# Kernel tuning notes

Hardware: AMD Instinct MI355X
Metric: run time of the kernel (lower is better)

The kernel has to match this reference:

```python
import jax, jax.numpy as jnp
import numpy as np

# Config (matches init_kwargs)
B, S, D = 1, 2048, 1024
H, KH, HD = 8, 2, 128          # n_heads, n_kv_heads, head_dim
R = 64                         # lora_rank
WINDOWS = [256, 512, 1024]
GLOBAL = 128
SCALE = HD ** -0.5
N_REP = H // KH


def _lora(x, w, a, b):
    # y = x @ w.T + (x @ A.T) @ B.T / rank
    return x @ w.T + (x @ a.T) @ b.T * (1.0 / R)


def _rope(x, cs):
    # x: [b, s, h, d]; cs: [s, d//2, 2] (cos, sin) -> complex rotation per pair
    b, s, h, d = x.shape
    xr = x.reshape(b, s, h, d // 2, 2)
    cos = cs[None, :, None, :, 0]
    sin = cs[None, :, None, :, 1]
    x1, x2 = xr[..., 0], xr[..., 1]
    out = jnp.stack([x1 * cos - x2 * sin, x1 * sin + x2 * cos], axis=-1)
    return out.reshape(b, s, h, d)


def _sparse_masks(q_len, k_len):
    aq = jnp.arange(q_len)
    ak = jnp.arange(k_len)
    diff = jnp.abs(ak[None, :] - aq[:, None])
    m = jnp.stack([(diff <= w // 2).astype(jnp.float32) for w in WINDOWS])  # [nw,q,k]
    return m.at[:, :, :GLOBAL].set(1.0)


def setup_inputs() -> dict:
    key = jax.random.key(0)
    ks = jax.random.split(key, 16)
    init = lambda k, shape: (jax.random.normal(k, shape, jnp.float32) * 0.02)
    return {
        "x": jax.random.normal(ks[0], (B, S, D), jnp.float32),
        "freqs_cis": jax.random.normal(ks[1], (S, HD // 2, 2), jnp.float32),
        "wq_w": init(ks[2], (H * HD, D)), "wq_a": init(ks[3], (R, D)), "wq_b": init(ks[4], (H * HD, R)),
        "wk_w": init(ks[5], (KH * HD, D)), "wk_a": init(ks[6], (R, D)), "wk_b": init(ks[7], (KH * HD, R)),
        "wv_w": init(ks[8], (KH * HD, D)), "wv_a": init(ks[9], (R, D)), "wv_b": init(ks[10], (KH * HD, R)),
        "wo_w": init(ks[11], (D, H * HD)), "wo_a": init(ks[12], (R, H * HD)), "wo_b": init(ks[13], (D, R)),
        "scale_weights": jnp.ones((len(WINDOWS),), jnp.float32),
        "start_pos": 0,
    }


def reference(x, freqs_cis, wq_w, wq_a, wq_b, wk_w, wk_a, wk_b, wv_w, wv_a, wv_b,
              wo_w, wo_a, wo_b, scale_weights, start_pos):
    bsz, seqlen, _ = x.shape
    xq = _lora(x, wq_w, wq_a, wq_b).reshape(bsz, seqlen, H, HD)
    xk = _lora(x, wk_w, wk_a, wk_b).reshape(bsz, seqlen, KH, HD)
    xv = _lora(x, wv_w, wv_a, wv_b).reshape(bsz, seqlen, KH, HD)
    cs = freqs_cis[start_pos:start_pos + seqlen]
    xq = _rope(xq, cs)
    xk = _rope(xk, cs)
    # no kv_cache: key/value = current xk/xv, repeated for GQA
    key = jnp.repeat(xk, N_REP, axis=2)    # [b,k,H,hd]
    value = jnp.repeat(xv, N_REP, axis=2)
    scores = jnp.einsum('bqhd,bkhd->bhqk', xq, key) * SCALE       # [b,H,q,k]
    masks = _sparse_masks(seqlen, key.shape[1])                    # [nw,q,k]
    multi_scores = scores[:, None] - (1.0 - masks)[None, :, None] * 10000.0  # [b,nw,H,q,k]
    multi_attn = jax.nn.softmax(multi_scores, axis=-1)
    w = jax.nn.softmax(scale_weights)[None, :, None, None, None]
    attn = (multi_attn * w).sum(axis=1)                            # [b,H,q,k]
    out = jnp.einsum('bhqk,bkhd->bqhd', attn, value).reshape(bsz, seqlen, H * HD)
    return _lora(out, wo_w, wo_a, wo_b)
```

## Files before the change

### kernel.cpp

```cpp
#include <hip/hip_runtime.h>
#include <hip/hip_bf16.h>
#include <cstdint>

#define S_LEN   2048
#define DMODEL  1024
#define NHEAD   8
#define HD      128
#define QSCALE  (0.08838834764831845f * 1.4426950408889634f)
#define THR2    11.5416f

typedef __attribute__((ext_vector_type(8))) short  bf16x8;
typedef __attribute__((ext_vector_type(4))) float  f32x4;

typedef __attribute__((address_space(1))) const unsigned int gu32;
typedef __attribute__((address_space(3))) unsigned int       lu32;

static __device__ __forceinline__ unsigned short f2bf(float x) {
  union { float f; unsigned u; } c; c.f = x;
  unsigned u = c.u + 0x7fff + ((c.u >> 16) & 1);
  return (unsigned short)(u >> 16);
}
static __device__ __forceinline__ f32x4 fz4() {
  f32x4 v; v[0] = 0.f; v[1] = 0.f; v[2] = 0.f; v[3] = 0.f; return v;
}

__global__ __launch_bounds__(256) void xcvt_kernel(
    const float* __restrict__ X, unsigned short* __restrict__ Xb)
{
  const int i = blockIdx.x * 256 + threadIdx.x;
  const float4 v = ((const float4*)X)[i];
  ushort4 o;
  o.x = f2bf(v.x); o.y = f2bf(v.y); o.z = f2bf(v.z); o.w = f2bf(v.w);
  ((ushort4*)Xb)[i] = o;
}

__global__ __launch_bounds__(256) void fuse_all_kernel(
    const float* __restrict__ wq_w, const float* __restrict__ wq_a, const float* __restrict__ wq_b,
    const float* __restrict__ wk_w, const float* __restrict__ wk_a, const float* __restrict__ wk_b,
    const float* __restrict__ wv_w, const float* __restrict__ wv_a, const float* __restrict__ wv_b,
    const float* __restrict__ wo_w, const float* __restrict__ wo_a, const float* __restrict__ wo_b,
    unsigned short* __restrict__ Wqkv, unsigned short* __restrict__ Wo)
{
  __shared__ float bs[64];
  const int t = threadIdx.x;
  const int o = blockIdx.x;
  const float *w, *a, *b; unsigned short* out; int ol;
  if (o < 1024)      { w = wq_w; a = wq_a; b = wq_b; out = Wqkv;              ol = o; }
  else if (o < 1280) { w = wk_w; a = wk_a; b = wk_b; out = Wqkv + 1024*1024;  ol = o - 1024; }
  else if (o < 1536) { w = wv_w; a = wv_a; b = wv_b; out = Wqkv + 1280*1024;  ol = o - 1280; }
  else               { w = wo_w; a = wo_a; b = wo_b; out = Wo;                ol = o - 1536; }
  if (t < 64) bs[t] = b[(size_t)ol * 64 + t];
  __syncthreads();
  float4 acc = {0.f, 0.f, 0.f, 0.f};
#pragma unroll 8
  for (int r = 0; r < 64; ++r) {
    const float4 av = *(const float4*)(a + (size_t)r * 1024 + t * 4);
    const float br = bs[r];
    acc.x += br * av.x; acc.y += br * av.y; acc.z += br * av.z; acc.w += br * av.w;
  }
  const float4 wv = *(const float4*)(w + (size_t)ol * 1024 + t * 4);
  ushort4 ov;
  ov.x = f2bf(wv.x + acc.x * 0.015625f);
  ov.y = f2bf(wv.y + acc.y * 0.015625f);
  ov.z = f2bf(wv.z + acc.z * 0.015625f);
  ov.w = f2bf(wv.w + acc.w * 0.015625f);
  *(ushort4*)(out + (size_t)ol * 1024 + t * 4) = ov;
}

template<int HEADMAJOR>
__global__ __launch_bounds__(256) void gemm_bf16(
    const unsigned short* __restrict__ A, const unsigned short* __restrict__ B,
    float* __restrict__ Y, int M, int N, int K)
{
  __shared__ __align__(16) unsigned short lds[2][(64 + 128) * 64];
  const int t = threadIdx.x;
  const int l = t & 63, wid = t >> 6;
  const int lr = l & 15, lq = l >> 4;
  const int m0 = blockIdx.y * 64, n0 = blockIdx.x * 128;
  const int wm = (wid >> 1) * 32, wn = (wid & 1) * 64;

  f32x4 acc[2][4];
#pragma unroll
  for (int i = 0; i < 2; ++i)
#pragma unroll
    for (int j = 0; j < 4; ++j) acc[i][j] = fz4();

  auto stage = [&](int buf, int k0) {
#pragma unroll
    for (int i = 0; i < 6; ++i) {
      const int ch = wid * 6 + i;
      const unsigned short* src;
      unsigned short* dst;
      int row;
      if (ch < 8) {
        row = ch * 8 + (l >> 3);
        src = A + (size_t)(m0 + row) * K + k0;
        dst = &lds[buf][ch * 512];
      } else {
        const int bh = ch - 8;
        row = bh * 8 + (l >> 3);
        src = B + (size_t)(n0 + row) * K + k0;
        dst = &lds[buf][4096 + bh * 512];
      }
      const int cg = (l & 7) ^ (row & 7);
      __builtin_amdgcn_global_load_lds((gu32*)(src + cg * 8), (lu32*)dst, 16, 0, 0);
    }
  };

  auto compute = [&](int buf) {
    const unsigned short* la = &lds[buf][0];
    const unsigned short* lb = &lds[buf][4096];
    bf16x8 af[2][2], bfr[4][2];
#pragma unroll
    for (int mi = 0; mi < 2; ++mi)
#pragma unroll
      for (int c = 0; c < 2; ++c) {
        const int row = wm + mi * 16 + lr;
        const int ck = (c * 4 + lq) ^ (row & 7);
        af[mi][c] = *(const bf16x8*)(la + row * 64 + ck * 8);
      }
#pragma unroll
    for (int nj = 0; nj < 4; ++nj)
#pragma unroll
      for (int c = 0; c < 2; ++c) {
        const int row = wn + nj * 16 + lr;
        const int ck = (c * 4 + lq) ^ (row & 7);
        bfr[nj][c] = *(const bf16x8*)(lb + row * 64 + ck * 8);
      }
#pragma unroll
    for (int c = 0; c < 2; ++c)
#pragma unroll
      for (int mi = 0; mi < 2; ++mi)
#pragma unroll
        for (int nj = 0; nj < 4; ++nj)
          acc[mi][nj] = __builtin_amdgcn_mfma_f32_16x16x32_bf16(
              af[mi][c], bfr[nj][c], acc[mi][nj], 0, 0, 0);
  };

  const int NT = K >> 6;
  stage(0, 0);
  int cur = 0;
#pragma unroll 1
  for (int kt = 0; kt < NT; ++kt) {
    __syncthreads();
    if (kt + 1 < NT) stage(cur ^ 1, (kt + 1) << 6);
    compute(cur);
    cur ^= 1;
  }

#pragma unroll
  for (int mi = 0; mi < 2; ++mi)
#pragma unroll
    for (int nj = 0; nj < 4; ++nj)
#pragma unroll
      for (int r = 0; r < 4; ++r) {
        const int row = m0 + wm + mi * 16 + lq * 4 + r;
        const int col = n0 + wn + nj * 16 + lr;
        if (HEADMAJOR)
          Y[(((size_t)(col >> 7) * M + row) << 7) + (col & 127)] = acc[mi][nj][r];
        else
          Y[(size_t)row * N + col] = acc[mi][nj][r];
      }
}

__global__ __launch_bounds__(256) void rope_cvt_kernel(
    const float* __restrict__ QKV, const float* __restrict__ fc,
    const int* __restrict__ sp,
    unsigned short* __restrict__ Qb, unsigned short* __restrict__ Kb)
{
  const int idx = blockIdx.x * 256 + threadIdx.x;
  const int i   = idx & 63;
  const int s   = (idx >> 6) & (S_LEN - 1);
  const int sec = idx >> 17;
  const float2 v  = *(const float2*)(QKV + ((size_t)sec * S_LEN + s) * 128 + 2 * i);
  const float2 cs = *(const float2*)(fc + (size_t)(sp[0] + s) * 128 + 2 * i);
  float xr = v.x * cs.x - v.y * cs.y;
  float yr = v.x * cs.y + v.y * cs.x;
  if (sec < 8) { xr *= QSCALE; yr *= QSCALE; }
  const unsigned w = (unsigned)f2bf(xr) | ((unsigned)f2bf(yr) << 16);
  if (sec < 8)
    ((unsigned*)Qb)[(((size_t)sec * S_LEN + s) * 128 + 2 * i) >> 1] = w;
  else
    ((unsigned*)Kb)[(((size_t)(sec - 8) * S_LEN + s) * 128 + 2 * i) >> 1] = w;
}

__global__ __launch_bounds__(256) void vtrans_kernel(
    const float* __restrict__ QKV, unsigned short* __restrict__ Vt)
{
  __shared__ float T[64][68];
  const int t = threadIdx.x;
  const int b = blockIdx.x;
  const int dt = b & 1, st = (b >> 1) & 31, kh = b >> 6;
  const int s0 = st * 64, d0 = dt * 64;
  const float* src = QKV + ((size_t)(10 + kh) * S_LEN + s0) * 128 + d0;
  const int row = t >> 4, c4 = (t & 15) * 4;
#pragma unroll
  for (int i = 0; i < 4; ++i) {
    const float4 v = *(const float4*)(src + (size_t)(row + i * 16) * 128 + c4);
    *(float4*)&T[row + i * 16][c4] = v;
  }
  __syncthreads();
  const int dl = t >> 2, s4 = (t & 3) * 16;
  unsigned short* dst = Vt + ((size_t)(kh * 128 + d0 + dl)) * S_LEN + s0 + s4;
#pragma unroll
  for (int half = 0; half < 2; ++half) {
    union { unsigned short u[8]; uint4 q; } o;
#pragma unroll
    for (int jj = 0; jj < 8; ++jj) o.u[jj] = f2bf(T[s4 + half * 8 + jj][dl]);
    *(uint4*)(dst + half * 8) = o.q;
  }
}

__global__ __launch_bounds__(128, 2) void attn_kernel(
    const unsigned short* __restrict__ Qb,
    const unsigned short* __restrict__ Kb,
    const unsigned short* __restrict__ Vt,
    const float* __restrict__ swp,
    unsigned short* __restrict__ AO)
{
  __shared__ __align__(16) unsigned short P[2][512];
  __shared__ __align__(16) float OS[6144];
  __shared__ float ST[3][16];
  __shared__ float MW;

  const int t   = threadIdx.x;
  const int wid = t >> 6;
  const int l   = t & 63;
  const int lr  = l & 15, lq = l >> 4;
  const int h   = blockIdx.y;
  const int q0  = blockIdx.x << 4;
  const int kvh = h >> 2;

  const unsigned short* Kp = Kb + (size_t)kvh * S_LEN * 128;
  const unsigned short* Vp = Vt + (size_t)kvh * 128 * S_LEN;

  bf16x8 qf[4];
#pragma unroll
  for (int c = 0; c < 4; ++c)
    qf[c] = *(const bf16x8*)(Qb + ((size_t)(h * S_LEN + q0 + lr)) * 128 + c * 32 + lq * 8);

  f32x4 o0[8], o1[8], o2[8];
#pragma unroll
  for (int i = 0; i < 8; ++i) { o0[i] = fz4(); o1[i] = fz4(); o2[i] = fz4(); }
  float sA[4], sB[4], sC[4];
#pragma unroll
  for (int r = 0; r < 4; ++r) { sA[r] = 0.f; sB[r] = 0.f; sC[r] = 0.f; }
  float M = -1e30f;

  const int t0w = (q0 >= 512) ? ((q0 - 512) >> 5) : 0;
  const int t1w = min(63, (q0 + 527) >> 5);
  int nA, base;
  if (t0w < 4) { nA = 0; base = 0; }
  else         { nA = 4; base = t0w; }
  const int n  = nA + t1w - base + 1;
  const int nh = n >> 1;
  const int jb = wid ? nh : 0;
  const int je = wid ? n  : nh;

#pragma unroll 1
  for (int j = jb; j < je; ++j) {
    const int tt = (j < nA) ? j : (base + j - nA);
    const int k0 = tt << 5;

    f32x4 s0 = fz4(), s1 = fz4();
#pragma unroll
    for (int c = 0; c < 4; ++c) {
      bf16x8 kf0 = *(const bf16x8*)(Kp + (size_t)(k0 + lr) * 128 + c * 32 + lq * 8);
      s0 = __builtin_amdgcn_mfma_f32_16x16x32_bf16(qf[c], kf0, s0, 0, 0, 0);
    }
#pragma unroll
    for (int c = 0; c < 4; ++c) {
      bf16x8 kf1 = *(const bf16x8*)(Kp + (size_t)(k0 + 16 + lr) * 128 + c * 32 + lq * 8);
      s1 = __builtin_amdgcn_mfma_f32_16x16x32_bf16(qf[c], kf1, s1, 0, 0, 0);
    }

    const int dminT = k0 - (q0 + 15);
    const int dmaxT = k0 + 31 - q0;
    const int aminT = (dminT <= 0 && dmaxT >= 0) ? 0 : min(::abs(dminT), ::abs(dmaxT));
    const int amaxT = max(::abs(dminT), ::abs(dmaxT));
    const int bminT = aminT <= 128 ? 0 : aminT <= 256 ? 1 : aminT <= 512 ? 2 : 3;
    const int bmaxT = amaxT <= 128 ? 0 : amaxT <= 256 ? 1 : amaxT <= 512 ? 2 : 3;
    const bool unifA = (k0 < 128);
    const bool unif  = unifA || (bminT == bmaxT);
    const int  ucls  = unifA ? 0 : bminT;

    float lm = fmaxf(s0[0], s1[0]);
#pragma unroll
    for (int r = 1; r < 4; ++r) lm = fmaxf(lm, fmaxf(s0[r], s1[r]));
    if (__any(lm > M + THR2)) {
      float wm = lm;
      wm = fmaxf(wm, __shfl_xor(wm, 1, 64));
      wm = fmaxf(wm, __shfl_xor(wm, 2, 64));
      wm = fmaxf(wm, __shfl_xor(wm, 4, 64));
      wm = fmaxf(wm, __shfl_xor(wm, 8, 64));
      wm = fmaxf(wm, __shfl_xor(wm, 16, 64));
      wm = fmaxf(wm, __shfl_xor(wm, 32, 64));
      const float Mn = fmaxf(M, wm);
      const float sc = __builtin_amdgcn_exp2f(M - Mn);
      M = Mn;
#pragma unroll
      for (int r = 0; r < 4; ++r) { sA[r] *= sc; sB[r] *= sc; sC[r] *= sc; }
#pragma unroll
      for (int db = 0; db < 8; ++db) { o0[db] *= sc; o1[db] *= sc; o2[db] *= sc; }
    }

    float p0[4], p1[4];
    int c0[4], c1[4];
#pragma unroll
    for (int r = 0; r < 4; ++r) {
      float e0 = __builtin_amdgcn_exp2f(s0[r] - M);
      float e1 = __builtin_amdgcn_exp2f(s1[r] - M);
      if (unif) {
        c0[r] = ucls; c1[r] = ucls;
        if (ucls == 0)      sA[r] += e0 + e1;
        else if (ucls == 1) sB[r] += e0 + e1;
        else                sC[r] += e0 + e1;
      } else {
        const int q  = q0 + lq * 4 + r;
        const int a0 = ::abs(k0 + lr - q);
        const int a1 = ::abs(k0 + 16 + lr - q);
        c0[r] = a0 <= 128 ? 0 : a0 <= 256 ? 1 : a0 <= 512 ? 2 : 3;
        c1[r] = a1 <= 128 ? 0 : a1 <= 256 ? 1 : a1 <= 512 ? 2 : 3;
        if (c0[r] == 3) e0 = 0.f;
        if (c1[r] == 3) e1 = 0.f;
        if (c0[r] == 0) sA[r] += e0; else if (c0[r] == 1) sB[r] += e0; else if (c0[r] == 2) sC[r] += e0;
        if (c1[r] == 0) sA[r] += e1; else if (c1[r] == 1) sB[r] += e1; else if (c1[r] == 2) sC[r] += e1;
      }
      p0[r] = e0; p1[r] = e1;
    }

    bf16x8 vf[8];
#pragma unroll
    for (int db = 0; db < 8; ++db)
      vf[db] = *(const bf16x8*)(Vp + (size_t)(db * 16 + lr) * S_LEN + k0 + lq * 8);

    if (unif) {
#pragma unroll
      for (int r = 0; r < 4; ++r) {
        const int q = lq * 4 + r;
        P[wid][q * 32 + (((lr >> 3) ^ r) << 3) + (lr & 7)]        = f2bf(p0[r]);
        P[wid][q * 32 + ((((16 + lr) >> 3) ^ r) << 3) + (lr & 7)] = f2bf(p1[r]);
      }
      const bf16x8 pa = *(const bf16x8*)&P[wid][lr * 32 + ((lq ^ (lr & 3)) << 3)];
      if (ucls == 0) {
#pragma unroll
        for (int db = 0; db < 8; ++db)
          o0[db] = __builtin_amdgcn_mfma_f32_16x16x32_bf16(pa, vf[db], o0[db], 0, 0, 0);
      } else if (ucls == 1) {
#pragma unroll
        for (int db = 0; db < 8; ++db)
          o1[db] = __builtin_amdgcn_mfma_f32_16x16x32_bf16(pa, vf[db], o1[db], 0, 0, 0);
      } else {
#pragma unroll
        for (int db = 0; db < 8; ++db)
          o2[db] = __builtin_amdgcn_mfma_f32_16x16x32_bf16(pa, vf[db], o2[db], 0, 0, 0);
      }
    } else {
#pragma unroll 1
      for (int pass = 0; pass < 2; ++pass) {
        const int cc = (pass == 0) ? bminT : bmaxT;
        if (cc == 3) continue;
#pragma unroll
        for (int r = 0; r < 4; ++r) {
          const int q = lq * 4 + r;
          const float u0 = (c0[r] == cc) ? p0[r] : 0.f;
          const float u1 = (c1[r] == cc) ? p1[r] : 0.f;
          P[wid][q * 32 + (((lr >> 3) ^ r) << 3) + (lr & 7)]        = f2bf(u0);
          P[wid][q * 32 + ((((16 + lr) >> 3) ^ r) << 3) + (lr & 7)] = f2bf(u1);
        }
        const bf16x8 pa = *(const bf16x8*)&P[wid][lr * 32 + ((lq ^ (lr & 3)) << 3)];
        if (cc == 0) {
#pragma unroll
          for (int db = 0; db < 8; ++db)
            o0[db] = __builtin_amdgcn_mfma_f32_16x16x32_bf16(pa, vf[db], o0[db], 0, 0, 0);
        } else if (cc == 1) {
#pragma unroll
          for (int db = 0; db < 8; ++db)
            o1[db] = __builtin_amdgcn_mfma_f32_16x16x32_bf16(pa, vf[db], o1[db], 0, 0, 0);
        } else {
#pragma unroll
          for (int db = 0; db < 8; ++db)
            o2[db] = __builtin_amdgcn_mfma_f32_16x16x32_bf16(pa, vf[db], o2[db], 0, 0, 0);
        }
      }
    }
  }

#pragma unroll
  for (int r = 0; r < 4; ++r) {
    sA[r] += __shfl_xor(sA[r], 1, 64); sA[r] += __shfl_xor(sA[r], 2, 64);
    sA[r] += __shfl_xor(sA[r], 4, 64); sA[r] += __shfl_xor(sA[r], 8, 64);
    sB[r] += __shfl_xor(sB[r], 1, 64); sB[r] += __shfl_xor(sB[r], 2, 64);
    sB[r] += __shfl_xor(sB[r], 4, 64); sB[r] += __shfl_xor(sB[r], 8, 64);
    sC[r] += __shfl_xor(sC[r], 1, 64); sC[r] += __shfl_xor(sC[r], 2, 64);
    sC[r] += __shfl_xor(sC[r], 4, 64); sC[r] += __shfl_xor(sC[r], 8, 64);
  }

  if (wid == 1) {
    if (l == 0) MW = M;
    if (lr == 0) {
#pragma unroll
      for (int r = 0; r < 4; ++r) {
        ST[0][lq * 4 + r] = sA[r];
        ST[1][lq * 4 + r] = sB[r];
        ST[2][lq * 4 + r] = sC[r];
      }
    }
#pragma unroll
    for (int db = 0; db < 8; ++db)
#pragma unroll
      for (int r = 0; r < 4; ++r) {
        OS[((0 * 8 + db) * 4 + r) * 64 + l] = o0[db][r];
        OS[((1 * 8 + db) * 4 + r) * 64 + l] = o1[db][r];
        OS[((2 * 8 + db) * 4 + r) * 64 + l] = o2[db][r];
      }
  }
  __syncthreads();
  if (wid == 1) return;

  {
    const float M1 = MW;
    const float Mn = fmaxf(M, M1);
    const float f0 = __builtin_amdgcn_exp2f(M - Mn);
    const float f1 = __builtin_amdgcn_exp2f(M1 - Mn);
#pragma unroll
    for (int r = 0; r < 4; ++r) {
      sA[r] = f0 * sA[r] + f1 * ST[0][lq * 4 + r];
      sB[r] = f0 * sB[r] + f1 * ST[1][lq * 4 + r];
      sC[r] = f0 * sC[r] + f1 * ST[2][lq * 4 + r];
    }
#pragma unroll
    for (int db = 0; db < 8; ++db)
#pragma unroll
      for (int r = 0; r < 4; ++r) {
        o0[db][r] = f0 * o0[db][r] + f1 * OS[((0 * 8 + db) * 4 + r) * 64 + l];
        o1[db][r] = f0 * o1[db][r] + f1 * OS[((1 * 8 + db) * 4 + r) * 64 + l];
        o2[db][r] = f0 * o2[db][r] + f1 * OS[((2 * 8 + db) * 4 + r) * 64 + l];
      }
  }

  const float w0 = swp[0], w1 = swp[1], w2 = swp[2];
  const float mw = fmaxf(w0, fmaxf(w1, w2));
  const float e0 = __expf(w0 - mw), e1 = __expf(w1 - mw), e2 = __expf(w2 - mw);
  const float inv = 1.f / (e0 + e1 + e2);
  const float g0 = e0 * inv, g1 = e1 * inv, g2 = e2 * inv;

#pragma unroll
  for (int r = 0; r < 4; ++r) {
    const float Z1 = sA[r], Z2 = Z1 + sB[r], Z3 = Z2 + sC[r];
    const float cC = g2 / Z3;
    const float cB = g1 / Z2 + cC;
    const float cA = g0 / Z1 + cB;
#pragma unroll
    for (int db = 0; db < 8; ++db)
      OS[(lq * 4 + r) * 132 + db * 16 + lr] =
          o0[db][r] * cA + o1[db][r] * cB + o2[db][r] * cC;
  }

  const int qr = l >> 2, dc = (l & 3) * 8;
  unsigned short* dst = AO + (size_t)(q0 + qr) * DMODEL + h * HD + dc;
#pragma unroll
  for (int j = 0; j < 4; ++j) {
    const float4 v0 = *(const float4*)&OS[qr * 132 + dc + j * 32];
    const float4 v1 = *(const float4*)&OS[qr * 132 + dc + j * 32 + 4];
    union { unsigned short u[8]; uint4 q4; } pk;
    pk.u[0] = f2bf(v0.x); pk.u[1] = f2bf(v0.y); pk.u[2] = f2bf(v0.z); pk.u[3] = f2bf(v0.w);
    pk.u[4] = f2bf(v1.x); pk.u[5] = f2bf(v1.y); pk.u[6] = f2bf(v1.z); pk.u[7] = f2bf(v1.w);
    *(uint4*)(dst + j * 32) = pk.q4;
  }
}

extern "C" void kernel_launch(void* const* d_in, const int* in_sizes, int n_in,
                              void* d_out, int out_size, void* d_ws, size_t ws_size,
                              hipStream_t stream) {
  const float* x    = (const float*)d_in[0];
  const float* fc   = (const float*)d_in[1];
  const float* wq_w = (const float*)d_in[2];
  const float* wq_a = (const float*)d_in[3];
  const float* wq_b = (const float*)d_in[4];
  const float* wk_w = (const float*)d_in[5];
  const float* wk_a = (const float*)d_in[6];
  const float* wk_b = (const float*)d_in[7];
  const float* wv_w = (const float*)d_in[8];
  const float* wv_a = (const float*)d_in[9];
  const float* wv_b = (const float*)d_in[10];
  const float* wo_w = (const float*)d_in[11];
  const float* wo_a = (const float*)d_in[12];
  const float* wo_b = (const float*)d_in[13];
  const float* sw   = (const float*)d_in[14];
  const int*   sp   = (const int*)d_in[15];
  float* out = (float*)d_out;

  char* wsb = (char*)d_ws;
  unsigned short* Wqkv = (unsigned short*)(wsb + 0);
  unsigned short* Wo   = (unsigned short*)(wsb + 3145728);
  unsigned short* Xbf  = (unsigned short*)(wsb + 5242880);
  float*          QKV  = (float*)(wsb + 9437184);
  unsigned short* Qb   = (unsigned short*)(wsb + 22020096);
  unsigned short* Kb   = (unsigned short*)(wsb + 26214400);
  unsigned short* Vt   = (unsigned short*)(wsb + 27262976);
  unsigned short* AO   = (unsigned short*)(wsb + 5242880);

  xcvt_kernel<<<2048, 256, 0, stream>>>(x, Xbf);
  fuse_all_kernel<<<2560, 256, 0, stream>>>(
      wq_w, wq_a, wq_b, wk_w, wk_a, wk_b, wv_w, wv_a, wv_b, wo_w, wo_a, wo_b,
      Wqkv, Wo);

  gemm_bf16<1><<<dim3(12, 32), 256, 0, stream>>>(Xbf, Wqkv, QKV, 2048, 1536, 1024);

  rope_cvt_kernel<<<5120, 256, 0, stream>>>(QKV, fc, sp, Qb, Kb);
  vtrans_kernel<<<128, 256, 0, stream>>>(QKV, Vt);

  attn_kernel<<<dim3(128, 8), 128, 0, stream>>>(Qb, Kb, Vt, sw, AO);

  gemm_bf16<0><<<dim3(8, 32), 256, 0, stream>>>(AO, Wo, out, 2048, 1024, 1024);
}
```

Measured before the change: 221.0 us.

## Two-pass attention with four-wave split, tiled LoRA fusion, smaller GEMM tiles

The attention kernel now uses four waves instead of two and runs two passes. The first pass finds the global row max and the per-window softmax denominators. The second pass folds the window-mixing coefficients into P, so only one O accumulator is kept instead of three, and a cheap LDS sum combines the waves. The LoRA weight-fusion kernel is re-tiled so each block computes a 64x128 output tile from shared-memory copies of A and B, cutting redundant global reads of A. The GEMM tile shrinks from 64x128 to 64x64 to launch more blocks; the costs are recomputing QK^T in the second pass and lower per-block reuse in the GEMM.

```diff
diff --git a/kernel.cpp b/kernel.cpp
--- a/kernel.cpp
+++ b/kernel.cpp
@@ -41,30 +41,62 @@
     const float* __restrict__ wo_w, const float* __restrict__ wo_a, const float* __restrict__ wo_b,
     unsigned short* __restrict__ Wqkv, unsigned short* __restrict__ Wo)
 {
-  __shared__ float bs[64];
-  const int t = threadIdx.x;
-  const int o = blockIdx.x;
-  const float *w, *a, *b; unsigned short* out; int ol;
-  if (o < 1024)      { w = wq_w; a = wq_a; b = wq_b; out = Wqkv;              ol = o; }
-  else if (o < 1280) { w = wk_w; a = wk_a; b = wk_b; out = Wqkv + 1024*1024;  ol = o - 1024; }
-  else if (o < 1536) { w = wv_w; a = wv_a; b = wv_b; out = Wqkv + 1280*1024;  ol = o - 1280; }
-  else               { w = wo_w; a = wo_a; b = wo_b; out = Wo;                ol = o - 1536; }
-  if (t < 64) bs[t] = b[(size_t)ol * 64 + t];
-  __syncthreads();
-  float4 acc = {0.f, 0.f, 0.f, 0.f};
-#pragma unroll 8
-  for (int r = 0; r < 64; ++r) {
-    const float4 av = *(const float4*)(a + (size_t)r * 1024 + t * 4);
-    const float br = bs[r];
-    acc.x += br * av.x; acc.y += br * av.y; acc.z += br * av.z; acc.w += br * av.w;
-  }
-  const float4 wv = *(const float4*)(w + (size_t)ol * 1024 + t * 4);
-  ushort4 ov;
-  ov.x = f2bf(wv.x + acc.x * 0.015625f);
-  ov.y = f2bf(wv.y + acc.y * 0.015625f);
-  ov.z = f2bf(wv.z + acc.z * 0.015625f);
-  ov.w = f2bf(wv.w + acc.w * 0.015625f);
-  *(ushort4*)(out + (size_t)ol * 1024 + t * 4) = ov;
+  __shared__ float bs[64][65];
+  __shared__ float as[16][132];
+  const int t  = threadIdx.x;
+  const int cb = blockIdx.x & 7, rb = blockIdx.x >> 3;
+  const int o0 = rb * 64;
+  const float *w, *a, *b; unsigned short* outp; int ob;
+  if (o0 < 1024)      { w = wq_w; a = wq_a; b = wq_b; outp = Wqkv;             ob = o0; }
+  else if (o0 < 1280) { w = wk_w; a = wk_a; b = wk_b; outp = Wqkv + 1024*1024; ob = o0 - 1024; }
+  else if (o0 < 1536) { w = wv_w; a = wv_a; b = wv_b; outp = Wqkv + 1280*1024; ob = o0 - 1280; }
+  else                { w = wo_w; a = wo_a; b = wo_b; outp = Wo;               ob = o0 - 1536; }
+
+#pragma unroll
+  for (int i = 0; i < 4; ++i) {
+    const int rr = (t >> 4) + i * 16, cc = (t & 15) * 4;
+    *(float4*)&bs[rr][cc] = *(const float4*)(b + (size_t)(ob + rr) * 64 + cc);
+  }
+
+  const int c0 = cb * 128;
+  const int tr = t >> 5;
+  const int co = (t & 31) * 4;
+  float4 ac[8];
+#pragma unroll
+  for (int i = 0; i < 8; ++i) ac[i] = {0.f, 0.f, 0.f, 0.f};
+
+#pragma unroll 1
+  for (int r0 = 0; r0 < 64; r0 += 16) {
+    __syncthreads();
+#pragma unroll
+    for (int i = 0; i < 2; ++i) {
+      const int rr = (t >> 5) + i * 8, cc = (t & 31) * 4;
+      *(float4*)&as[rr][cc] = *(const float4*)(a + (size_t)(r0 + rr) * 1024 + c0 + cc);
+    }
+    __syncthreads();
+#pragma unroll
+    for (int rr = 0; rr < 16; ++rr) {
+      const float4 av = *(const float4*)&as[rr][co];
+#pragma unroll
+      for (int ri = 0; ri < 8; ++ri) {
+        const float bv = bs[tr * 8 + ri][r0 + rr];
+        ac[ri].x += bv * av.x; ac[ri].y += bv * av.y;
+        ac[ri].z += bv * av.z; ac[ri].w += bv * av.w;
+      }
+    }
+  }
+
+#pragma unroll
+  for (int ri = 0; ri < 8; ++ri) {
+    const int row = tr * 8 + ri;
+    const float4 wv = *(const float4*)(w + (size_t)(ob + row) * 1024 + c0 + co);
+    ushort4 ov;
+    ov.x = f2bf(wv.x + ac[ri].x * 0.015625f);
+    ov.y = f2bf(wv.y + ac[ri].y * 0.015625f);
+    ov.z = f2bf(wv.z + ac[ri].z * 0.015625f);
+    ov.w = f2bf(wv.w + ac[ri].w * 0.015625f);
+    *(ushort4*)(outp + (size_t)(ob + row) * 1024 + c0 + co) = ov;
+  }
 }
 
 template<int HEADMAJOR>
@@ -72,23 +104,23 @@
     const unsigned short* __restrict__ A, const unsigned short* __restrict__ B,
     float* __restrict__ Y, int M, int N, int K)
 {
-  __shared__ __align__(16) unsigned short lds[2][(64 + 128) * 64];
+  __shared__ __align__(16) unsigned short lds[2][128 * 64];
   const int t = threadIdx.x;
   const int l = t & 63, wid = t >> 6;
   const int lr = l & 15, lq = l >> 4;
-  const int m0 = blockIdx.y * 64, n0 = blockIdx.x * 128;
-  const int wm = (wid >> 1) * 32, wn = (wid & 1) * 64;
-
-  f32x4 acc[2][4];
+  const int m0 = blockIdx.y * 64, n0 = blockIdx.x * 64;
+  const int wm = (wid >> 1) * 32, wn = (wid & 1) * 32;
+
+  f32x4 acc[2][2];
 #pragma unroll
   for (int i = 0; i < 2; ++i)
 #pragma unroll
-    for (int j = 0; j < 4; ++j) acc[i][j] = fz4();
+    for (int j = 0; j < 2; ++j) acc[i][j] = fz4();
 
   auto stage = [&](int buf, int k0) {
 #pragma unroll
-    for (int i = 0; i < 6; ++i) {
-      const int ch = wid * 6 + i;
+    for (int i = 0; i < 4; ++i) {
+      const int ch = wid * 4 + i;
       const unsigned short* src;
       unsigned short* dst;
       int row;
@@ -97,10 +129,9 @@
         src = A + (size_t)(m0 + row) * K + k0;
         dst = &lds[buf][ch * 512];
       } else {
-        const int bh = ch - 8;
-        row = bh * 8 + (l >> 3);
+        row = (ch - 8) * 8 + (l >> 3);
         src = B + (size_t)(n0 + row) * K + k0;
-        dst = &lds[buf][4096 + bh * 512];
+        dst = &lds[buf][ch * 512];
       }
       const int cg = (l & 7) ^ (row & 7);
       __builtin_amdgcn_global_load_lds((gu32*)(src + cg * 8), (lu32*)dst, 16, 0, 0);
@@ -110,7 +141,7 @@
   auto compute = [&](int buf) {
     const unsigned short* la = &lds[buf][0];
     const unsigned short* lb = &lds[buf][4096];
-    bf16x8 af[2][2], bfr[4][2];
+    bf16x8 af[2][2], bfr[2][2];
 #pragma unroll
     for (int mi = 0; mi < 2; ++mi)
 #pragma unroll
@@ -120,7 +151,7 @@
         af[mi][c] = *(const bf16x8*)(la + row * 64 + ck * 8);
       }
 #pragma unroll
-    for (int nj = 0; nj < 4; ++nj)
+    for (int nj = 0; nj < 2; ++nj)
 #pragma unroll
       for (int c = 0; c < 2; ++c) {
         const int row = wn + nj * 16 + lr;
@@ -132,7 +163,7 @@
 #pragma unroll
       for (int mi = 0; mi < 2; ++mi)
 #pragma unroll
-        for (int nj = 0; nj < 4; ++nj)
+        for (int nj = 0; nj < 2; ++nj)
           acc[mi][nj] = __builtin_amdgcn_mfma_f32_16x16x32_bf16(
               af[mi][c], bfr[nj][c], acc[mi][nj], 0, 0, 0);
   };
@@ -151,7 +182,7 @@
 #pragma unroll
   for (int mi = 0; mi < 2; ++mi)
 #pragma unroll
-    for (int nj = 0; nj < 4; ++nj)
+    for (int nj = 0; nj < 2; ++nj)
 #pragma unroll
       for (int r = 0; r < 4; ++r) {
         const int row = m0 + wm + mi * 16 + lq * 4 + r;
@@ -211,21 +242,20 @@
   }
 }
 
-__global__ __launch_bounds__(128, 2) void attn_kernel(
+__global__ __launch_bounds__(256, 3) void attn_kernel(
     const unsigned short* __restrict__ Qb,
     const unsigned short* __restrict__ Kb,
     const unsigned short* __restrict__ Vt,
     const float* __restrict__ swp,
     unsigned short* __restrict__ AO)
 {
-  __shared__ __align__(16) unsigned short P[2][512];
-  __shared__ __align__(16) float OS[6144];
-  __shared__ float ST[3][16];
-  __shared__ float MW;
+  __shared__ __align__(16) unsigned short P[4][512];
+  __shared__ float OS[4][32][65];
+  __shared__ float ST[4][3][16];
+  __shared__ float MB[4];
 
   const int t   = threadIdx.x;
-  const int wid = t >> 6;
-  const int l   = t & 63;
+  const int wid = t >> 6, l = t & 63;
   const int lr  = l & 15, lq = l >> 4;
   const int h   = blockIdx.y;
   const int q0  = blockIdx.x << 4;
@@ -238,14 +268,6 @@
 #pragma unroll
   for (int c = 0; c < 4; ++c)
     qf[c] = *(const bf16x8*)(Qb + ((size_t)(h * S_LEN + q0 + lr)) * 128 + c * 32 + lq * 8);
-
-  f32x4 o0[8], o1[8], o2[8];
-#pragma unroll
-  for (int i = 0; i < 8; ++i) { o0[i] = fz4(); o1[i] = fz4(); o2[i] = fz4(); }
-  float sA[4], sB[4], sC[4];
-#pragma unroll
-  for (int r = 0; r < 4; ++r) { sA[r] = 0.f; sB[r] = 0.f; sC[r] = 0.f; }
-  float M = -1e30f;
 
   const int t0w = (q0 >= 512) ? ((q0 - 512) >> 5) : 0;
   const int t1w = min(63, (q0 + 527) >> 5);
@@ -253,136 +275,83 @@
   if (t0w < 4) { nA = 0; base = 0; }
   else         { nA = 4; base = t0w; }
   const int n  = nA + t1w - base + 1;
-  const int nh = n >> 1;
-  const int jb = wid ? nh : 0;
-  const int je = wid ? n  : nh;
-
-#pragma unroll 1
-  for (int j = jb; j < je; ++j) {
-    const int tt = (j < nA) ? j : (base + j - nA);
-    const int k0 = tt << 5;
-
-    f32x4 s0 = fz4(), s1 = fz4();
-#pragma unroll
-    for (int c = 0; c < 4; ++c) {
-      bf16x8 kf0 = *(const bf16x8*)(Kp + (size_t)(k0 + lr) * 128 + c * 32 + lq * 8);
-      s0 = __builtin_amdgcn_mfma_f32_16x16x32_bf16(qf[c], kf0, s0, 0, 0, 0);
-    }
-#pragma unroll
-    for (int c = 0; c < 4; ++c) {
-      bf16x8 kf1 = *(const bf16x8*)(Kp + (size_t)(k0 + 16 + lr) * 128 + c * 32 + lq * 8);
-      s1 = __builtin_amdgcn_mfma_f32_16x16x32_bf16(qf[c], kf1, s1, 0, 0, 0);
-    }
-
-    const int dminT = k0 - (q0 + 15);
-    const int dmaxT = k0 + 31 - q0;
-    const int aminT = (dminT <= 0 && dmaxT >= 0) ? 0 : min(::abs(dminT), ::abs(dmaxT));
-    const int amaxT = max(::abs(dminT), ::abs(dmaxT));
-    const int bminT = aminT <= 128 ? 0 : aminT <= 256 ? 1 : aminT <= 512 ? 2 : 3;
-    const int bmaxT = amaxT <= 128 ? 0 : amaxT <= 256 ? 1 : amaxT <= 512 ? 2 : 3;
-    const bool unifA = (k0 < 128);
-    const bool unif  = unifA || (bminT == bmaxT);
-    const int  ucls  = unifA ? 0 : bminT;
-
-    float lm = fmaxf(s0[0], s1[0]);
-#pragma unroll
-    for (int r = 1; r < 4; ++r) lm = fmaxf(lm, fmaxf(s0[r], s1[r]));
-    if (__any(lm > M + THR2)) {
-      float wm = lm;
-      wm = fmaxf(wm, __shfl_xor(wm, 1, 64));
-      wm = fmaxf(wm, __shfl_xor(wm, 2, 64));
-      wm = fmaxf(wm, __shfl_xor(wm, 4, 64));
-      wm = fmaxf(wm, __shfl_xor(wm, 8, 64));
-      wm = fmaxf(wm, __shfl_xor(wm, 16, 64));
-      wm = fmaxf(wm, __shfl_xor(wm, 32, 64));
-      const float Mn = fmaxf(M, wm);
-      const float sc = __builtin_amdgcn_exp2f(M - Mn);
-      M = Mn;
-#pragma unroll
-      for (int r = 0; r < 4; ++r) { sA[r] *= sc; sB[r] *= sc; sC[r] *= sc; }
-#pragma unroll
-      for (int db = 0; db < 8; ++db) { o0[db] *= sc; o1[db] *= sc; o2[db] *= sc; }
-    }
-
-    float p0[4], p1[4];
-    int c0[4], c1[4];
-#pragma unroll
-    for (int r = 0; r < 4; ++r) {
-      float e0 = __builtin_amdgcn_exp2f(s0[r] - M);
-      float e1 = __builtin_amdgcn_exp2f(s1[r] - M);
-      if (unif) {
-        c0[r] = ucls; c1[r] = ucls;
-        if (ucls == 0)      sA[r] += e0 + e1;
-        else if (ucls == 1) sB[r] += e0 + e1;
-        else                sC[r] += e0 + e1;
-      } else {
-        const int q  = q0 + lq * 4 + r;
-        const int a0 = ::abs(k0 + lr - q);
-        const int a1 = ::abs(k0 + 16 + lr - q);
-        c0[r] = a0 <= 128 ? 0 : a0 <= 256 ? 1 : a0 <= 512 ? 2 : 3;
-        c1[r] = a1 <= 128 ? 0 : a1 <= 256 ? 1 : a1 <= 512 ? 2 : 3;
-        if (c0[r] == 3) e0 = 0.f;
-        if (c1[r] == 3) e1 = 0.f;
-        if (c0[r] == 0) sA[r] += e0; else if (c0[r] == 1) sB[r] += e0; else if (c0[r] == 2) sC[r] += e0;
-        if (c1[r] == 0) sA[r] += e1; else if (c1[r] == 1) sB[r] += e1; else if (c1[r] == 2) sC[r] += e1;
-      }
-      p0[r] = e0; p1[r] = e1;
-    }
-
-    bf16x8 vf[8];
-#pragma unroll
-    for (int db = 0; db < 8; ++db)
-      vf[db] = *(const bf16x8*)(Vp + (size_t)(db * 16 + lr) * S_LEN + k0 + lq * 8);
-
-    if (unif) {
-#pragma unroll
-      for (int r = 0; r < 4; ++r) {
-        const int q = lq * 4 + r;
-        P[wid][q * 32 + (((lr >> 3) ^ r) << 3) + (lr & 7)]        = f2bf(p0[r]);
-        P[wid][q * 32 + ((((16 + lr) >> 3) ^ r) << 3) + (lr & 7)] = f2bf(p1[r]);
-      }
-      const bf16x8 pa = *(const bf16x8*)&P[wid][lr * 32 + ((lq ^ (lr & 3)) << 3)];
-      if (ucls == 0) {
-#pragma unroll
-        for (int db = 0; db < 8; ++db)
-          o0[db] = __builtin_amdgcn_mfma_f32_16x16x32_bf16(pa, vf[db], o0[db], 0, 0, 0);
-      } else if (ucls == 1) {
-#pragma unroll
-        for (int db = 0; db < 8; ++db)
-          o1[db] = __builtin_amdgcn_mfma_f32_16x16x32_bf16(pa, vf[db], o1[db], 0, 0, 0);
-      } else {
-#pragma unroll
-        for (int db = 0; db < 8; ++db)
-          o2[db] = __builtin_amdgcn_mfma_f32_16x16x32_bf16(pa, vf[db], o2[db], 0, 0, 0);
-      }
-    } else {
-#pragma unroll 1
-      for (int pass = 0; pass < 2; ++pass) {
-        const int cc = (pass == 0) ? bminT : bmaxT;
-        if (cc == 3) continue;
-#pragma unroll
-        for (int r = 0; r < 4; ++r) {
-          const int q = lq * 4 + r;
-          const float u0 = (c0[r] == cc) ? p0[r] : 0.f;
-          const float u1 = (c1[r] == cc) ? p1[r] : 0.f;
-          P[wid][q * 32 + (((lr >> 3) ^ r) << 3) + (lr & 7)]        = f2bf(u0);
-          P[wid][q * 32 + ((((16 + lr) >> 3) ^ r) << 3) + (lr & 7)] = f2bf(u1);
-        }
-        const bf16x8 pa = *(const bf16x8*)&P[wid][lr * 32 + ((lq ^ (lr & 3)) << 3)];
-        if (cc == 0) {
-#pragma unroll
-          for (int db = 0; db < 8; ++db)
-            o0[db] = __builtin_amdgcn_mfma_f32_16x16x32_bf16(pa, vf[db], o0[db], 0, 0, 0);
-        } else if (cc == 1) {
-#pragma unroll
-          for (int db = 0; db < 8; ++db)
-            o1[db] = __builtin_amdgcn_mfma_f32_16x16x32_bf16(pa, vf[db], o1[db], 0, 0, 0);
-        } else {
-#pragma unroll
-          for (int db = 0; db < 8; ++db)
-            o2[db] = __builtin_amdgcn_mfma_f32_16x16x32_bf16(pa, vf[db], o2[db], 0, 0, 0);
-        }
-      }
+  const int jb = (n * wid) >> 2;
+  const int je = (n * (wid + 1)) >> 2;
+
+#define TILE(J) (((J) < nA) ? (J) : (base + (J) - nA))
+
+#define LOADK(DST, K0)                                                         \
+  { _Pragma("unroll") for (int c = 0; c < 4; ++c) {                            \
+      DST[c]     = *(const bf16x8*)(Kp + (size_t)((K0) + lr) * 128 + c * 32 + lq * 8);      \
+      DST[4 + c] = *(const bf16x8*)(Kp + (size_t)((K0) + 16 + lr) * 128 + c * 32 + lq * 8); \
+    } }
+
+  float sA[4], sB[4], sC[4];
+#pragma unroll
+  for (int r = 0; r < 4; ++r) { sA[r] = 0.f; sB[r] = 0.f; sC[r] = 0.f; }
+  float M = -1e30f;
+
+#define PASS1_TILE(KF)                                                         \
+  { const int k0 = tc << 5;                                                    \
+    f32x4 s0 = fz4(), s1 = fz4();                                              \
+    _Pragma("unroll") for (int c = 0; c < 4; ++c)                              \
+      s0 = __builtin_amdgcn_mfma_f32_16x16x32_bf16(qf[c], KF[c], s0, 0, 0, 0); \
+    _Pragma("unroll") for (int c = 0; c < 4; ++c)                              \
+      s1 = __builtin_amdgcn_mfma_f32_16x16x32_bf16(qf[c], KF[4 + c], s1, 0, 0, 0); \
+    const int dminT = k0 - (q0 + 15), dmaxT = k0 + 31 - q0;                    \
+    const int aminT = (dminT <= 0 && dmaxT >= 0) ? 0 : min(::abs(dminT), ::abs(dmaxT)); \
+    const int amaxT = max(::abs(dminT), ::abs(dmaxT));                         \
+    const int bminT = aminT <= 128 ? 0 : aminT <= 256 ? 1 : 2;                 \
+    const int bmaxT = amaxT <= 128 ? 0 : amaxT <= 256 ? 1 : amaxT <= 512 ? 2 : 3; \
+    const bool unif = (k0 < 128) || (bminT == bmaxT);                          \
+    const int  ucls = (k0 < 128) ? 0 : bminT;                                  \
+    float lm = fmaxf(fmaxf(s0[0], s1[0]), fmaxf(s0[1], s1[1]));                \
+    lm = fmaxf(lm, fmaxf(fmaxf(s0[2], s1[2]), fmaxf(s0[3], s1[3])));           \
+    if (__any(lm > M + THR2)) {                                                \
+      float wm = lm;                                                           \
+      wm = fmaxf(wm, __shfl_xor(wm, 1, 64));  wm = fmaxf(wm, __shfl_xor(wm, 2, 64)); \
+      wm = fmaxf(wm, __shfl_xor(wm, 4, 64));  wm = fmaxf(wm, __shfl_xor(wm, 8, 64)); \
+      wm = fmaxf(wm, __shfl_xor(wm, 16, 64)); wm = fmaxf(wm, __shfl_xor(wm, 32, 64)); \
+      const float Mn = fmaxf(M, wm);                                           \
+      const float sc = __builtin_amdgcn_exp2f(M - Mn);                         \
+      M = Mn;                                                                  \
+      _Pragma("unroll") for (int r = 0; r < 4; ++r) { sA[r] *= sc; sB[r] *= sc; sC[r] *= sc; } \
+    }                                                                          \
+    _Pragma("unroll") for (int r = 0; r < 4; ++r) {                            \
+      float e0 = __builtin_amdgcn_exp2f(s0[r] - M);                            \
+      float e1 = __builtin_amdgcn_exp2f(s1[r] - M);                            \
+      if (unif) {                                                              \
+        if (ucls == 0)      sA[r] += e0 + e1;                                  \
+        else if (ucls == 1) sB[r] += e0 + e1;                                  \
+        else                sC[r] += e0 + e1;                                  \
+      } else {                                                                 \
+        const int q  = q0 + lq * 4 + r;                                        \
+        const int a0 = ::abs(k0 + lr - q);                                     \
+        const int a1 = ::abs(k0 + 16 + lr - q);                                \
+        const int c0 = a0 <= 128 ? 0 : a0 <= 256 ? 1 : a0 <= 512 ? 2 : 3;      \
+        const int c1 = a1 <= 128 ? 0 : a1 <= 256 ? 1 : a1 <= 512 ? 2 : 3;      \
+        if (c0 == 0) sA[r] += e0; else if (c0 == 1) sB[r] += e0; else if (c0 == 2) sC[r] += e0; \
+        if (c1 == 0) sA[r] += e1; else if (c1 == 1) sB[r] += e1; else if (c1 == 2) sC[r] += e1; \
+      }                                                                        \
+    } }
+
+  {
+    bf16x8 kA[8], kB[8];
+    int j = jb, tc = TILE(jb);
+    LOADK(kA, tc << 5);
+    for (;;) {
+      { const int jn = j + 1; const bool hn = jn < je;
+        const int tn = hn ? TILE(jn) : tc;
+        if (hn) LOADK(kB, tn << 5);
+        PASS1_TILE(kA);
+        if (!hn) break;
+        j = jn; tc = tn; }
+      { const int jn = j + 1; const bool hn = jn < je;
+        const int tn = hn ? TILE(jn) : tc;
+        if (hn) LOADK(kA, tn << 5);
+        PASS1_TILE(kB);
+        if (!hn) break;
+        j = jn; tc = tn; }
     }
   }
 
@@ -395,79 +364,139 @@
     sC[r] += __shfl_xor(sC[r], 1, 64); sC[r] += __shfl_xor(sC[r], 2, 64);
     sC[r] += __shfl_xor(sC[r], 4, 64); sC[r] += __shfl_xor(sC[r], 8, 64);
   }
-
-  if (wid == 1) {
-    if (l == 0) MW = M;
-    if (lr == 0) {
-#pragma unroll
-      for (int r = 0; r < 4; ++r) {
-        ST[0][lq * 4 + r] = sA[r];
-        ST[1][lq * 4 + r] = sB[r];
-        ST[2][lq * 4 + r] = sC[r];
-      }
-    }
-#pragma unroll
-    for (int db = 0; db < 8; ++db)
-#pragma unroll
-      for (int r = 0; r < 4; ++r) {
-        OS[((0 * 8 + db) * 4 + r) * 64 + l] = o0[db][r];
-        OS[((1 * 8 + db) * 4 + r) * 64 + l] = o1[db][r];
-        OS[((2 * 8 + db) * 4 + r) * 64 + l] = o2[db][r];
-      }
-  }
+  if (lr == 0) {
+#pragma unroll
+    for (int r = 0; r < 4; ++r) {
+      ST[wid][0][lq * 4 + r] = sA[r];
+      ST[wid][1][lq * 4 + r] = sB[r];
+      ST[wid][2][lq * 4 + r] = sC[r];
+    }
+  }
+  if (l == 0) MB[wid] = M;
   __syncthreads();
-  if (wid == 1) return;
-
-  {
-    const float M1 = MW;
-    const float Mn = fmaxf(M, M1);
-    const float f0 = __builtin_amdgcn_exp2f(M - Mn);
-    const float f1 = __builtin_amdgcn_exp2f(M1 - Mn);
-#pragma unroll
-    for (int r = 0; r < 4; ++r) {
-      sA[r] = f0 * sA[r] + f1 * ST[0][lq * 4 + r];
-      sB[r] = f0 * sB[r] + f1 * ST[1][lq * 4 + r];
-      sC[r] = f0 * sC[r] + f1 * ST[2][lq * 4 + r];
-    }
-#pragma unroll
-    for (int db = 0; db < 8; ++db)
-#pragma unroll
-      for (int r = 0; r < 4; ++r) {
-        o0[db][r] = f0 * o0[db][r] + f1 * OS[((0 * 8 + db) * 4 + r) * 64 + l];
-        o1[db][r] = f0 * o1[db][r] + f1 * OS[((1 * 8 + db) * 4 + r) * 64 + l];
-        o2[db][r] = f0 * o2[db][r] + f1 * OS[((2 * 8 + db) * 4 + r) * 64 + l];
-      }
-  }
-
+
+  const float Ms = fmaxf(fmaxf(MB[0], MB[1]), fmaxf(MB[2], MB[3]));
+  const float fw0 = __builtin_amdgcn_exp2f(MB[0] - Ms);
+  const float fw1 = __builtin_amdgcn_exp2f(MB[1] - Ms);
+  const float fw2 = __builtin_amdgcn_exp2f(MB[2] - Ms);
+  const float fw3 = __builtin_amdgcn_exp2f(MB[3] - Ms);
   const float w0 = swp[0], w1 = swp[1], w2 = swp[2];
   const float mw = fmaxf(w0, fmaxf(w1, w2));
   const float e0 = __expf(w0 - mw), e1 = __expf(w1 - mw), e2 = __expf(w2 - mw);
   const float inv = 1.f / (e0 + e1 + e2);
   const float g0 = e0 * inv, g1 = e1 * inv, g2 = e2 * inv;
-
+  float cfA[4], cfB[4], cfC[4];
 #pragma unroll
   for (int r = 0; r < 4; ++r) {
-    const float Z1 = sA[r], Z2 = Z1 + sB[r], Z3 = Z2 + sC[r];
-    const float cC = g2 / Z3;
-    const float cB = g1 / Z2 + cC;
-    const float cA = g0 / Z1 + cB;
-#pragma unroll
-    for (int db = 0; db < 8; ++db)
-      OS[(lq * 4 + r) * 132 + db * 16 + lr] =
-          o0[db][r] * cA + o1[db][r] * cB + o2[db][r] * cC;
-  }
-
-  const int qr = l >> 2, dc = (l & 3) * 8;
-  unsigned short* dst = AO + (size_t)(q0 + qr) * DMODEL + h * HD + dc;
-#pragma unroll
-  for (int j = 0; j < 4; ++j) {
-    const float4 v0 = *(const float4*)&OS[qr * 132 + dc + j * 32];
-    const float4 v1 = *(const float4*)&OS[qr * 132 + dc + j * 32 + 4];
-    union { unsigned short u[8]; uint4 q4; } pk;
-    pk.u[0] = f2bf(v0.x); pk.u[1] = f2bf(v0.y); pk.u[2] = f2bf(v0.z); pk.u[3] = f2bf(v0.w);
-    pk.u[4] = f2bf(v1.x); pk.u[5] = f2bf(v1.y); pk.u[6] = f2bf(v1.z); pk.u[7] = f2bf(v1.w);
-    *(uint4*)(dst + j * 32) = pk.q4;
-  }
+    const int q = lq * 4 + r;
+    const float ZA = ST[0][0][q] * fw0 + ST[1][0][q] * fw1 + ST[2][0][q] * fw2 + ST[3][0][q] * fw3;
+    const float ZB = ST[0][1][q] * fw0 + ST[1][1][q] * fw1 + ST[2][1][q] * fw2 + ST[3][1][q] * fw3;
+    const float ZC = ST[0][2][q] * fw0 + ST[1][2][q] * fw1 + ST[2][2][q] * fw2 + ST[3][2][q] * fw3;
+    const float Z1 = ZA, Z2 = Z1 + ZB, Z3 = Z2 + ZC;
+    const float cC_ = g2 / Z3;
+    const float cB_ = g1 / Z2 + cC_;
+    const float cA_ = g0 / Z1 + cB_;
+    cfA[r] = cA_; cfB[r] = cB_; cfC[r] = cC_;
+  }
+
+  f32x4 o[8];
+#pragma unroll
+  for (int i = 0; i < 8; ++i) o[i] = fz4();
+
+#pragma unroll 1
+  for (int j = jb; j < je; ++j) {
+    const int tt = TILE(j);
+    const int k0 = tt << 5;
+
+    bf16x8 vf0, vf1, vf2, vf3;
+    vf0 = *(const bf16x8*)(Vp + (size_t)(0 * 16 + lr) * S_LEN + k0 + lq * 8);
+    vf1 = *(const bf16x8*)(Vp + (size_t)(1 * 16 + lr) * S_LEN + k0 + lq * 8);
+    vf2 = *(const bf16x8*)(Vp + (size_t)(2 * 16 + lr) * S_LEN + k0 + lq * 8);
+    vf3 = *(const bf16x8*)(Vp + (size_t)(3 * 16 + lr) * S_LEN + k0 + lq * 8);
+
+    bf16x8 kA[8];
+    LOADK(kA, k0);
+    f32x4 s0 = fz4(), s1 = fz4();
+#pragma unroll
+    for (int c = 0; c < 4; ++c)
+      s0 = __builtin_amdgcn_mfma_f32_16x16x32_bf16(qf[c], kA[c], s0, 0, 0, 0);
+#pragma unroll
+    for (int c = 0; c < 4; ++c)
+      s1 = __builtin_amdgcn_mfma_f32_16x16x32_bf16(qf[c], kA[4 + c], s1, 0, 0, 0);
+
+    const int dminT = k0 - (q0 + 15), dmaxT = k0 + 31 - q0;
+    const int aminT = (dminT <= 0 && dmaxT >= 0) ? 0 : min(::abs(dminT), ::abs(dmaxT));
+    const int amaxT = max(::abs(dminT), ::abs(dmaxT));
+    const int bminT = aminT <= 128 ? 0 : aminT <= 256 ? 1 : 2;
+    const int bmaxT = amaxT <= 128 ? 0 : amaxT <= 256 ? 1 : amaxT <= 512 ? 2 : 3;
+    const bool unif = (k0 < 128) || (bminT == bmaxT);
+    const int  ucls = (k0 < 128) ? 0 : bminT;
+
+    float p0[4], p1[4];
+#pragma unroll
+    for (int r = 0; r < 4; ++r) {
+      const float ee0 = __builtin_amdgcn_exp2f(s0[r] - Ms);
+      const float ee1 = __builtin_amdgcn_exp2f(s1[r] - Ms);
+      float co0, co1;
+      if (unif) {
+        co0 = (ucls == 0) ? cfA[r] : (ucls == 1) ? cfB[r] : cfC[r];
+        co1 = co0;
+      } else {
+        const int q  = q0 + lq * 4 + r;
+        const int a0 = ::abs(k0 + lr - q);
+        const int a1 = ::abs(k0 + 16 + lr - q);
+        const int c0 = a0 <= 128 ? 0 : a0 <= 256 ? 1 : a0 <= 512 ? 2 : 3;
+        const int c1 = a1 <= 128 ? 0 : a1 <= 256 ? 1 : a1 <= 512 ? 2 : 3;
+        co0 = (c0 == 0) ? cfA[r] : (c0 == 1) ? cfB[r] : (c0 == 2) ? cfC[r] : 0.f;
+        co1 = (c1 == 0) ? cfA[r] : (c1 == 1) ? cfB[r] : (c1 == 2) ? cfC[r] : 0.f;
+      }
+      p0[r] = ee0 * co0;
+      p1[r] = ee1 * co1;
+    }
+
+#pragma unroll
+    for (int r = 0; r < 4; ++r) {
+      const int q = lq * 4 + r;
+      P[wid][q * 32 + (((lr >> 3) ^ r) << 3) + (lr & 7)]        = f2bf(p0[r]);
+      P[wid][q * 32 + ((((16 + lr) >> 3) ^ r) << 3) + (lr & 7)] = f2bf(p1[r]);
+    }
+    const bf16x8 pa = *(const bf16x8*)&P[wid][lr * 32 + ((lq ^ (lr & 3)) << 3)];
+
+    o[0] = __builtin_amdgcn_mfma_f32_16x16x32_bf16(pa, vf0, o[0], 0, 0, 0);
+    o[1] = __builtin_amdgcn_mfma_f32_16x16x32_bf16(pa, vf1, o[1], 0, 0, 0);
+    o[2] = __builtin_amdgcn_mfma_f32_16x16x32_bf16(pa, vf2, o[2], 0, 0, 0);
+    o[3] = __builtin_amdgcn_mfma_f32_16x16x32_bf16(pa, vf3, o[3], 0, 0, 0);
+
+    bf16x8 vg0, vg1, vg2, vg3;
+    vg0 = *(const bf16x8*)(Vp + (size_t)(4 * 16 + lr) * S_LEN + k0 + lq * 8);
+    vg1 = *(const bf16x8*)(Vp + (size_t)(5 * 16 + lr) * S_LEN + k0 + lq * 8);
+    vg2 = *(const bf16x8*)(Vp + (size_t)(6 * 16 + lr) * S_LEN + k0 + lq * 8);
+    vg3 = *(const bf16x8*)(Vp + (size_t)(7 * 16 + lr) * S_LEN + k0 + lq * 8);
+    o[4] = __builtin_amdgcn_mfma_f32_16x16x32_bf16(pa, vg0, o[4], 0, 0, 0);
+    o[5] = __builtin_amdgcn_mfma_f32_16x16x32_bf16(pa, vg1, o[5], 0, 0, 0);
+    o[6] = __builtin_amdgcn_mfma_f32_16x16x32_bf16(pa, vg2, o[6], 0, 0, 0);
+    o[7] = __builtin_amdgcn_mfma_f32_16x16x32_bf16(pa, vg3, o[7], 0, 0, 0);
+  }
+
+#pragma unroll
+  for (int db = 0; db < 8; ++db)
+#pragma unroll
+    for (int r = 0; r < 4; ++r)
+      OS[wid][db * 4 + r][l] = o[db][r];
+  __syncthreads();
+
+  const int qr = t >> 4, dc = (t & 15) * 8;
+  const int db2 = dc >> 4, dlo = dc & 15;
+  const int row = db2 * 4 + (qr & 3);
+  const int colb = (qr >> 2) * 16 + dlo;
+  union { unsigned short u[8]; uint4 q4; } pk;
+#pragma unroll
+  for (int jj = 0; jj < 8; ++jj) {
+    const float v = OS[0][row][colb + jj] + OS[1][row][colb + jj] +
+                    OS[2][row][colb + jj] + OS[3][row][colb + jj];
+    pk.u[jj] = f2bf(v);
+  }
+  *(uint4*)(AO + (size_t)(q0 + qr) * DMODEL + h * HD + dc) = pk.q4;
 }
 
 extern "C" void kernel_launch(void* const* d_in, const int* in_sizes, int n_in,
@@ -502,16 +531,16 @@
   unsigned short* AO   = (unsigned short*)(wsb + 5242880);
 
   xcvt_kernel<<<2048, 256, 0, stream>>>(x, Xbf);
-  fuse_all_kernel<<<2560, 256, 0, stream>>>(
+  fuse_all_kernel<<<320, 256, 0, stream>>>(
       wq_w, wq_a, wq_b, wk_w, wk_a, wk_b, wv_w, wv_a, wv_b, wo_w, wo_a, wo_b,
       Wqkv, Wo);
 
-  gemm_bf16<1><<<dim3(12, 32), 256, 0, stream>>>(Xbf, Wqkv, QKV, 2048, 1536, 1024);
+  gemm_bf16<1><<<dim3(24, 32), 256, 0, stream>>>(Xbf, Wqkv, QKV, 2048, 1536, 1024);
 
   rope_cvt_kernel<<<5120, 256, 0, stream>>>(QKV, fc, sp, Qb, Kb);
   vtrans_kernel<<<128, 256, 0, stream>>>(QKV, Vt);
 
-  attn_kernel<<<dim3(128, 8), 128, 0, stream>>>(Qb, Kb, Vt, sw, AO);
-
-  gemm_bf16<0><<<dim3(8, 32), 256, 0, stream>>>(AO, Wo, out, 2048, 1024, 1024);
-}
+  attn_kernel<<<dim3(128, 8), 256, 0, stream>>>(Qb, Kb, Vt, sw, AO);
+
+  gemm_bf16<0><<<dim3(16, 32), 256, 0, stream>>>(AO, Wo, out, 2048, 1024, 1024);
+}
```

Measured after the change: 254.4 us. 15.1% more time.
